# Kernel tuning notes

Measured on AMD Instinct MI355X. Metric: run time of the kernel, lower is better.

The kernel has to match this reference:

```python
import jax, jax.numpy as jnp
import numpy as np
import math

M, N, D = 16384, 8192, 128
SIGMA = 1.0

def setup_inputs() -> dict:
    key = jax.random.key(0)
    k1, k2, k3 = jax.random.split(key, 3)
    x = jax.random.normal(k1, (M, D), dtype=jnp.float32)
    means = jax.random.normal(k2, (N, D), dtype=jnp.float32)
    weights = jax.random.uniform(k3, (N,), dtype=jnp.float32)
    return {"x": x, "means": means, "weights": weights}

def reference(x, means, weights):
    # GMM.eval_batch: cdist -> square -> gaussian kernel -> weighted sum
    var = SIGMA ** 2
    x = x.reshape(-1, means.shape[-1])
    x2 = jnp.sum(x * x, axis=-1, keepdims=True)            # (M,1)
    m2 = jnp.sum(means * means, axis=-1)                   # (N,)
    sq = jnp.maximum(x2 + m2[None, :] - 2.0 * (x @ means.T), 0.0)  # (M,N)
    coef = 1.0 / (2.0 * math.pi * var)
    dens = coef * jnp.exp(-sq / (2.0 * var))               # (M,N)
    return dens @ weights                                  # (M,)
```

## Files before the change

### kernel.cpp

```cpp
#include <hip/hip_runtime.h>
#include <math.h>

#define MM 16384
#define NN 8192
#define DD 128

#define L2E  1.4426950408889634f
#define COEF 0.15915494309189535f

__device__ __forceinline__ unsigned short f2h(float f) {
    _Float16 h = (_Float16)f;
    unsigned short u;
    __builtin_memcpy(&u, &h, 2);
    return u;
}

__device__ __forceinline__ void async16(short* lds, const short* g) {
    __builtin_amdgcn_global_load_lds(
        (const __attribute__((address_space(1))) unsigned int*)g,
        (__attribute__((address_space(3))) unsigned int*)lds,
        16, 0, 0);
}

typedef __attribute__((ext_vector_type(8))) _Float16 f16x8;
typedef __attribute__((ext_vector_type(4))) float f32x4;

__global__ __launch_bounds__(256) void gmm_prep_f16(
    const float* __restrict__ x, const float* __restrict__ means,
    const float* __restrict__ w, short* __restrict__ Acat,
    short* __restrict__ Bcat, float* __restrict__ xc, float* __restrict__ mc)
{
    const int tid  = threadIdx.x;
    const int rbk  = blockIdx.x;
    const bool isx = rbk < (MM / 16);
    const int rb   = isx ? rbk : rbk - (MM / 16);
    const int lane = tid & 63;
    const int rp   = (tid >> 6) * 4 + (lane >> 4);
    const int cg   = lane & 15;
    const int p    = cg >> 2;
    const int gk   = cg & 3;
    const int row  = rb * 16 + rp;

    const float* src = (isx ? x : means) + (size_t)row * DD + cg * 8;
    float4 u0 = ((const float4*)src)[0];
    float4 u1 = ((const float4*)src)[1];
    float a[8] = {u0.x, u0.y, u0.z, u0.w, u1.x, u1.y, u1.z, u1.w};

    float ss = 0.f;
    unsigned hi[4];
    #pragma unroll
    for (int q = 0; q < 4; ++q) {
        ss = fmaf(a[2 * q], a[2 * q], fmaf(a[2 * q + 1], a[2 * q + 1], ss));
        float a0 = isx ? a[2 * q] * L2E     : a[2 * q];
        float a1 = isx ? a[2 * q + 1] * L2E : a[2 * q + 1];
        hi[q] = (unsigned)f2h(a0) | ((unsigned)f2h(a1) << 16);
    }
    uint4 HI = make_uint4(hi[0], hi[1], hi[2], hi[3]);

    const int slot = rp * 4 + ((gk + (rp >> 1)) & 3);
    short* base = (isx ? Acat : Bcat) + (size_t)rb * 2048 + p * 512 + slot * 8;
    *(uint4*)base = HI;

    ss += __shfl_xor(ss, 1, 16);
    ss += __shfl_xor(ss, 2, 16);
    ss += __shfl_xor(ss, 4, 16);
    ss += __shfl_xor(ss, 8, 16);
    if (cg == 0) {
        if (isx) xc[row] = -0.5f * ss * L2E;
        else     mc[row] = (logf(w[row]) - 0.5f * ss) * L2E;
    }
}

__global__ __launch_bounds__(512, 4) void gmm_mfma(
    const short* __restrict__ Acat, const short* __restrict__ Bcat,
    const float* __restrict__ xc, const float* __restrict__ mc,
    float* __restrict__ out)
{
    __shared__ __align__(16) short smem[36864];
    __shared__ float red[4][128];

#define AS(b) (smem + (b) * 4096)
#define BS(b) (smem + 12288 + (b) * 8192)

    const int tid  = threadIdx.x;
    const int w    = tid >> 6, lane = tid & 63;
    const int wm   = w >> 2,   wn   = w & 3;
    const int quad = lane >> 4, col = lane & 15;
    const int m0   = blockIdx.x * 128;
    const int nb   = blockIdx.y * 256;

    const short* ga  = Acat + (size_t)(blockIdx.x * 8 + w) * 2048 + lane * 8;
    const short* gb0 = Bcat + (size_t)(blockIdx.y * 16 + w * 2) * 2048 + lane * 8;
    const short* gb1 = gb0 + 2048;
    const int aofs  = w * 512;
    const int bofs0 = w * 1024;
    const int bofs1 = w * 1024 + 512;

    float mcv[4];
    #pragma unroll
    for (int j = 0; j < 4; ++j) mcv[j] = mc[nb + wn * 64 + j * 16 + col];
    float xa[4][4];
    #pragma unroll
    for (int i = 0; i < 4; ++i) {
        float4 xv = *(const float4*)(xc + m0 + wm * 64 + i * 16 + quad * 4);
        xa[i][0] = xv.x; xa[i][1] = xv.y; xa[i][2] = xv.z; xa[i][3] = xv.w;
    }

    f32x4 acc[4][4];
    #pragma unroll
    for (int i = 0; i < 4; ++i)
        #pragma unroll
        for (int j = 0; j < 4; ++j)
            acc[i][j] = (f32x4){xa[i][0] + mcv[j], xa[i][1] + mcv[j],
                                xa[i][2] + mcv[j], xa[i][3] + mcv[j]};

    asm volatile("s_waitcnt vmcnt(0)" ::: "memory");
    __builtin_amdgcn_sched_barrier(0);

    async16(AS(0) + aofs,  ga);
    async16(BS(0) + bofs0, gb0);
    async16(BS(0) + bofs1, gb1);
    async16(AS(1) + aofs,  ga  + 512);
    async16(BS(1) + bofs0, gb0 + 512);
    async16(BS(1) + bofs1, gb1 + 512);

    const int rdo = col * 32 + ((quad + (col >> 1)) & 3) * 8;

#define COMPUTE(as_, bs_)                                                     \
    {                                                                         \
        const short* as = (as_);                                              \
        const short* bs = (bs_);                                              \
        f16x8 af[4];                                                          \
        _Pragma("unroll")                                                     \
        for (int i = 0; i < 4; ++i)                                           \
            af[i] = *(const f16x8*)(as + (wm * 4 + i) * 512 + rdo);           \
        _Pragma("unroll")                                                     \
        for (int j = 0; j < 4; ++j) {                                         \
            f16x8 bfr = *(const f16x8*)(&bs[(wn * 4 + j) * 512 + rdo]);       \
            _Pragma("unroll")                                                 \
            for (int i = 0; i < 4; ++i)                                       \
                acc[i][j] = __builtin_amdgcn_mfma_f32_16x16x32_f16(           \
                    af[i], bfr, acc[i][j], 0, 0, 0);                          \
        }                                                                     \
    }

    asm volatile("s_waitcnt vmcnt(3)" ::: "memory");
    __builtin_amdgcn_sched_barrier(0);
    __builtin_amdgcn_s_barrier();
    __builtin_amdgcn_sched_barrier(0);
    async16(AS(2) + aofs,  ga  + 1024);
    async16(BS(2) + bofs0, gb0 + 1024);
    async16(BS(2) + bofs1, gb1 + 1024);
    COMPUTE(AS(0), BS(0));

    asm volatile("s_waitcnt vmcnt(3)" ::: "memory");
    __builtin_amdgcn_sched_barrier(0);
    __builtin_amdgcn_s_barrier();
    __builtin_amdgcn_sched_barrier(0);
    async16(AS(0) + aofs,  ga  + 1536);
    async16(BS(0) + bofs0, gb0 + 1536);
    async16(BS(0) + bofs1, gb1 + 1536);
    COMPUTE(AS(1), BS(1));

    asm volatile("s_waitcnt vmcnt(3)" ::: "memory");
    __builtin_amdgcn_sched_barrier(0);
    __builtin_amdgcn_s_barrier();
    __builtin_amdgcn_sched_barrier(0);
    COMPUTE(AS(2), BS(2));

    asm volatile("s_waitcnt vmcnt(0)" ::: "memory");
    __builtin_amdgcn_sched_barrier(0);
    __builtin_amdgcn_s_barrier();
    __builtin_amdgcn_sched_barrier(0);
    COMPUTE(AS(0), BS(0));
#undef COMPUTE

    float sv[4][4];
    #pragma unroll
    for (int i = 0; i < 4; ++i) {
        #pragma unroll
        for (int r = 0; r < 4; ++r) {
            float s = 0.f;
            #pragma unroll
            for (int j = 0; j < 4; ++j)
                s += __builtin_exp2f(acc[i][j][r]);
            sv[i][r] = s;
        }
    }
    __syncthreads();
    {
        float* S = (float*)smem;
        const int p = wn * 16 + col;
        #pragma unroll
        for (int i = 0; i < 4; ++i) {
            const int mb = wm * 64 + i * 16 + quad * 4;
            #pragma unroll
            for (int r = 0; r < 4; ++r)
                S[(mb + r) * 68 + p] = sv[i][r];
        }
    }
    __syncthreads();
    {
        const float* S = (const float*)smem;
        const int m  = tid & 127;
        const int pg = tid >> 7;
        const float4* v = (const float4*)(S + m * 68 + pg * 16);
        float4 a0 = v[0], a1 = v[1], a2 = v[2], a3 = v[3];
        red[pg][m] = (a0.x + a0.y + a0.z + a0.w) + (a1.x + a1.y + a1.z + a1.w)
                   + (a2.x + a2.y + a2.z + a2.w) + (a3.x + a3.y + a3.z + a3.w);
    }
    __syncthreads();
    if (tid < 128)
        atomicAdd(out + m0 + tid,
                  COEF * (red[0][tid] + red[1][tid] + red[2][tid] + red[3][tid]));
#undef AS
#undef BS
}

__global__ __launch_bounds__(256) void gmm_prep(
    const float* __restrict__ x, const float* __restrict__ means,
    const float* __restrict__ w, float* __restrict__ xc, float* __restrict__ mc)
{
    int tid = blockIdx.x * 256 + threadIdx.x;
    if (tid < MM) {
        const float4* row = (const float4*)(x + (size_t)tid * DD);
        float ss = 0.f;
        #pragma unroll
        for (int i = 0; i < DD / 4; ++i) {
            float4 v = row[i];
            ss = fmaf(v.x, v.x, fmaf(v.y, v.y, fmaf(v.z, v.z, fmaf(v.w, v.w, ss))));
        }
        xc[tid] = -0.5f * ss * L2E;
    } else if (tid < MM + NN) {
        int n = tid - MM;
        const float4* row = (const float4*)(means + (size_t)n * DD);
        float ss = 0.f;
        #pragma unroll
        for (int i = 0; i < DD / 4; ++i) {
            float4 v = row[i];
            ss = fmaf(v.x, v.x, fmaf(v.y, v.y, fmaf(v.z, v.z, fmaf(v.w, v.w, ss))));
        }
        mc[n] = (logf(w[n]) - 0.5f * ss) * L2E;
    }
}

__global__ __launch_bounds__(256, 2) void gmm_main(
    const float* __restrict__ x, const float* __restrict__ means,
    const float* __restrict__ xc, const float* __restrict__ mc,
    float* __restrict__ out)
{
    __shared__ __align__(16) float Asm[128 * 128];
    __shared__ __align__(16) float Bsm[2][16 * 128];

    const int t   = threadIdx.x;
    const int tc  = t & 15;
    const int tr  = t >> 4;
    const int r0  = blockIdx.x * 128;
    const int nq0 = blockIdx.y * 2048;

    {
        float4 tmp[16];
        #pragma unroll
        for (int ii = 0; ii < 16; ++ii) {
            int idx = t + ii * 256;
            int r   = idx >> 5;
            int k0  = (idx & 31) << 2;
            tmp[ii] = *(const float4*)(x + (size_t)(r0 + r) * DD + k0);
        }
        #pragma unroll
        for (int ii = 0; ii < 16; ++ii) {
            int idx = t + ii * 256;
            int r   = idx >> 5;
            int k0  = (idx & 31) << 2;
            int rb  = r >> 3, rl = r & 7;
            float v[4] = {tmp[ii].x, tmp[ii].y, tmp[ii].z, tmp[ii].w};
            #pragma unroll
            for (int j = 0; j < 4; ++j) {
                int k = k0 + j;
                Asm[k * 128 + (((rb ^ (k & 15)) << 3) | rl)] = v[j];
            }
        }
    }

    float xcv[8];
    {
        float4 a = *(const float4*)(xc + r0 + tr * 8);
        float4 b = *(const float4*)(xc + r0 + tr * 8 + 4);
        xcv[0] = a.x; xcv[1] = a.y; xcv[2] = a.z; xcv[3] = a.w;
        xcv[4] = b.x; xcv[5] = b.y; xcv[6] = b.z; xcv[7] = b.w;
    }

    float rowAcc[8];
    #pragma unroll
    for (int i = 0; i < 8; ++i) rowAcc[i] = 0.f;

    for (int ntile = 0; ntile < 16; ++ntile) {
        const int nbase = nq0 + ntile * 128;

        float acc[8][8];
        #pragma unroll
        for (int i = 0; i < 8; ++i)
            #pragma unroll
            for (int j = 0; j < 8; ++j) acc[i][j] = 0.f;

        float4 ld[2];
        #pragma unroll
        for (int ii = 0; ii < 2; ++ii) {
            int flat = t + ii * 256;
            int nl   = flat >> 2;
            int kl   = (flat & 3) << 2;
            ld[ii] = *(const float4*)(means + (size_t)(nbase + nl) * DD + kl);
        }

        for (int ks = 0; ks < 8; ++ks) {
            const int buf = ks & 1;
            #pragma unroll
            for (int ii = 0; ii < 2; ++ii) {
                int flat = t + ii * 256;
                int nl   = flat >> 2;
                int k0   = (flat & 3) << 2;
                int nbk  = nl >> 3, nll = nl & 7;
                float v[4] = {ld[ii].x, ld[ii].y, ld[ii].z, ld[ii].w};
                #pragma unroll
                for (int j = 0; j < 4; ++j) {
                    int kl = k0 + j;
                    Bsm[buf][kl * 128 + (((nbk ^ kl) << 3) | nll)] = v[j];
                }
            }
            if (ks < 7) {
                #pragma unroll
                for (int ii = 0; ii < 2; ++ii) {
                    int flat = t + ii * 256;
                    int nl   = flat >> 2;
                    int kl   = (flat & 3) << 2;
                    ld[ii] = *(const float4*)(means + (size_t)(nbase + nl) * DD
                                              + (ks + 1) * 16 + kl);
                }
            }
            __syncthreads();

            #pragma unroll
            for (int kk = 0; kk < 16; ++kk) {
                const int k = ks * 16 + kk;
                const float* apx = &Asm[k * 128 + ((tr ^ kk) << 3)];
                float4 a0 = *(const float4*)apx;
                float4 a1 = *(const float4*)(apx + 4);
                const float* bpx = &Bsm[buf][kk * 128 + ((tc ^ kk) << 3)];
                float4 b0 = *(const float4*)bpx;
                float4 b1 = *(const float4*)(bpx + 4);
                float av[8] = {a0.x, a0.y, a0.z, a0.w, a1.x, a1.y, a1.z, a1.w};
                float bv[8] = {b0.x, b0.y, b0.z, b0.w, b1.x, b1.y, b1.z, b1.w};
                #pragma unroll
                for (int i = 0; i < 8; ++i)
                    #pragma unroll
                    for (int j = 0; j < 8; ++j)
                        acc[i][j] = fmaf(av[i], bv[j], acc[i][j]);
            }
        }

        float mcv[8];
        {
            float4 a = *(const float4*)(mc + nbase + tc * 8);
            float4 b = *(const float4*)(mc + nbase + tc * 8 + 4);
            mcv[0] = a.x; mcv[1] = a.y; mcv[2] = a.z; mcv[3] = a.w;
            mcv[4] = b.x; mcv[5] = b.y; mcv[6] = b.z; mcv[7] = b.w;
        }
        #pragma unroll
        for (int i = 0; i < 8; ++i) {
            float s = 0.f;
            #pragma unroll
            for (int j = 0; j < 8; ++j) {
                float arg = fmaf(acc[i][j], L2E, xcv[i] + mcv[j]);
                s += __builtin_exp2f(arg);
            }
            rowAcc[i] += s;
        }
    }

    #pragma unroll
    for (int i = 0; i < 8; ++i) {
        float v = rowAcc[i];
        v += __shfl_xor(v, 1, 16);
        v += __shfl_xor(v, 2, 16);
        v += __shfl_xor(v, 4, 16);
        v += __shfl_xor(v, 8, 16);
        if (tc == 0) atomicAdd(out + r0 + tr * 8 + i, COEF * v);
    }
}

extern "C" void kernel_launch(void* const* d_in, const int* in_sizes, int n_in,
                              void* d_out, int out_size, void* d_ws, size_t ws_size,
                              hipStream_t stream) {
    const float* x     = (const float*)d_in[0];
    const float* means = (const float*)d_in[1];
    const float* w     = (const float*)d_in[2];
    float* out = (float*)d_out;

    const size_t needA = (size_t)MM * 128 * sizeof(short);
    const size_t needB = (size_t)NN * 128 * sizeof(short);
    const size_t need  = needA + needB + (size_t)(MM + NN) * 4;

    if (ws_size >= need) {
        short* Acat = (short*)d_ws;
        short* Bcat = Acat + (size_t)MM * 128;
        float* xc   = (float*)(Bcat + (size_t)NN * 128);
        float* mc   = xc + MM;
        hipMemsetAsync(out, 0, MM * sizeof(float), stream);
        gmm_prep_f16<<<(MM + NN) / 16, 256, 0, stream>>>(x, means, w, Acat, Bcat, xc, mc);
        gmm_mfma<<<dim3(MM / 128, NN / 256), 512, 0, stream>>>(Acat, Bcat, xc, mc, out);
    } else {
        float* xc = (float*)d_ws;
        float* mc = xc + MM;
        hipMemsetAsync(out, 0, MM * sizeof(float), stream);
        gmm_prep<<<(MM + NN + 255) / 256, 256, 0, stream>>>(x, means, w, xc, mc);
        gmm_main<<<dim3(MM / 128, 4), 256, 0, stream>>>(x, means, xc, mc, out);
    }
}
```

Baseline: 123.3 us.

## Shrink MFMA block tile to 128x128 with 256 threads and 4 waves

Changes the fused GEMM-exp kernel from a 128x256 tile with 8 waves to a 128x128 tile with 4 waves, so each wave now loads two A and two B chunks per stage. LDS use per block drops, the grid doubles along N, and the reduction is adjusted to two partial groups. The aim is more resident blocks per CU and better latency hiding. In exchange, B-tile reuse per block is lower, global and L2 traffic for A rises, and twice as many atomics go to the output.

```diff
diff --git a/kernel.cpp b/kernel.cpp
--- a/kernel.cpp
+++ b/kernel.cpp
@@ -71,30 +71,30 @@
     }
 }
 
-__global__ __launch_bounds__(512, 4) void gmm_mfma(
+__global__ __launch_bounds__(256, 3) void gmm_mfma(
     const short* __restrict__ Acat, const short* __restrict__ Bcat,
     const float* __restrict__ xc, const float* __restrict__ mc,
     float* __restrict__ out)
 {
-    __shared__ __align__(16) short smem[36864];
-    __shared__ float red[4][128];
+    __shared__ __align__(16) short smem[24576];
+    __shared__ float red[2][128];
 
 #define AS(b) (smem + (b) * 4096)
-#define BS(b) (smem + 12288 + (b) * 8192)
+#define BS(b) (smem + 12288 + (b) * 4096)
 
     const int tid  = threadIdx.x;
     const int w    = tid >> 6, lane = tid & 63;
-    const int wm   = w >> 2,   wn   = w & 3;
+    const int wm   = w >> 1,   wn   = w & 1;
     const int quad = lane >> 4, col = lane & 15;
     const int m0   = blockIdx.x * 128;
-    const int nb   = blockIdx.y * 256;
-
-    const short* ga  = Acat + (size_t)(blockIdx.x * 8 + w) * 2048 + lane * 8;
-    const short* gb0 = Bcat + (size_t)(blockIdx.y * 16 + w * 2) * 2048 + lane * 8;
+    const int nb   = blockIdx.y * 128;
+
+    const short* ga0 = Acat + (size_t)(blockIdx.x * 8 + w * 2) * 2048 + lane * 8;
+    const short* ga1 = ga0 + 2048;
+    const short* gb0 = Bcat + (size_t)(blockIdx.y * 8 + w * 2) * 2048 + lane * 8;
     const short* gb1 = gb0 + 2048;
-    const int aofs  = w * 512;
-    const int bofs0 = w * 1024;
-    const int bofs1 = w * 1024 + 512;
+    const int ofs0 = w * 1024;
+    const int ofs1 = w * 1024 + 512;
 
     float mcv[4];
     #pragma unroll
@@ -117,14 +117,22 @@
     asm volatile("s_waitcnt vmcnt(0)" ::: "memory");
     __builtin_amdgcn_sched_barrier(0);
 
-    async16(AS(0) + aofs,  ga);
-    async16(BS(0) + bofs0, gb0);
-    async16(BS(0) + bofs1, gb1);
-    async16(AS(1) + aofs,  ga  + 512);
-    async16(BS(1) + bofs0, gb0 + 512);
-    async16(BS(1) + bofs1, gb1 + 512);
+    async16(AS(0) + ofs0, ga0);
+    async16(AS(0) + ofs1, ga1);
+    async16(BS(0) + ofs0, gb0);
+    async16(BS(0) + ofs1, gb1);
+    async16(AS(1) + ofs0, ga0 + 512);
+    async16(AS(1) + ofs1, ga1 + 512);
+    async16(BS(1) + ofs0, gb0 + 512);
+    async16(BS(1) + ofs1, gb1 + 512);
 
     const int rdo = col * 32 + ((quad + (col >> 1)) & 3) * 8;
+
+#define ISSUE(G, B)                                                           \
+    async16(AS(B) + ofs0, ga0 + (G) * 512);                                   \
+    async16(AS(B) + ofs1, ga1 + (G) * 512);                                   \
+    async16(BS(B) + ofs0, gb0 + (G) * 512);                                   \
+    async16(BS(B) + ofs1, gb1 + (G) * 512);
 
 #define COMPUTE(as_, bs_)                                                     \
     {                                                                         \
@@ -144,25 +152,21 @@
         }                                                                     \
     }
 
-    asm volatile("s_waitcnt vmcnt(3)" ::: "memory");
+    asm volatile("s_waitcnt vmcnt(4)" ::: "memory");
     __builtin_amdgcn_sched_barrier(0);
     __builtin_amdgcn_s_barrier();
     __builtin_amdgcn_sched_barrier(0);
-    async16(AS(2) + aofs,  ga  + 1024);
-    async16(BS(2) + bofs0, gb0 + 1024);
-    async16(BS(2) + bofs1, gb1 + 1024);
+    ISSUE(2, 2)
     COMPUTE(AS(0), BS(0));
 
-    asm volatile("s_waitcnt vmcnt(3)" ::: "memory");
+    asm volatile("s_waitcnt vmcnt(4)" ::: "memory");
     __builtin_amdgcn_sched_barrier(0);
     __builtin_amdgcn_s_barrier();
     __builtin_amdgcn_sched_barrier(0);
-    async16(AS(0) + aofs,  ga  + 1536);
-    async16(BS(0) + bofs0, gb0 + 1536);
-    async16(BS(0) + bofs1, gb1 + 1536);
+    ISSUE(3, 0)
     COMPUTE(AS(1), BS(1));
 
-    asm volatile("s_waitcnt vmcnt(3)" ::: "memory");
+    asm volatile("s_waitcnt vmcnt(4)" ::: "memory");
     __builtin_amdgcn_sched_barrier(0);
     __builtin_amdgcn_s_barrier();
     __builtin_amdgcn_sched_barrier(0);
@@ -173,6 +177,7 @@
     __builtin_amdgcn_s_barrier();
     __builtin_amdgcn_sched_barrier(0);
     COMPUTE(AS(0), BS(0));
+#undef ISSUE
 #undef COMPUTE
 
     float sv[4][4];
@@ -196,7 +201,7 @@
             const int mb = wm * 64 + i * 16 + quad * 4;
             #pragma unroll
             for (int r = 0; r < 4; ++r)
-                S[(mb + r) * 68 + p] = sv[i][r];
+                S[(mb + r) * 36 + p] = sv[i][r];
         }
     }
     __syncthreads();
@@ -204,15 +209,14 @@
         const float* S = (const float*)smem;
         const int m  = tid & 127;
         const int pg = tid >> 7;
-        const float4* v = (const float4*)(S + m * 68 + pg * 16);
+        const float4* v = (const float4*)(S + m * 36 + pg * 16);
         float4 a0 = v[0], a1 = v[1], a2 = v[2], a3 = v[3];
         red[pg][m] = (a0.x + a0.y + a0.z + a0.w) + (a1.x + a1.y + a1.z + a1.w)
                    + (a2.x + a2.y + a2.z + a2.w) + (a3.x + a3.y + a3.z + a3.w);
     }
     __syncthreads();
     if (tid < 128)
-        atomicAdd(out + m0 + tid,
-                  COEF * (red[0][tid] + red[1][tid] + red[2][tid] + red[3][tid]));
+        atomicAdd(out + m0 + tid, COEF * (red[0][tid] + red[1][tid]));
 #undef AS
 #undef BS
 }
@@ -407,7 +411,7 @@
         float* mc   = xc + MM;
         hipMemsetAsync(out, 0, MM * sizeof(float), stream);
         gmm_prep_f16<<<(MM + NN) / 16, 256, 0, stream>>>(x, means, w, Acat, Bcat, xc, mc);
-        gmm_mfma<<<dim3(MM / 128, NN / 256), 512, 0, stream>>>(Acat, Bcat, xc, mc, out);
+        gmm_mfma<<<dim3(MM / 128, NN / 128), 256, 0, stream>>>(Acat, Bcat, xc, mc, out);
     } else {
         float* xc = (float*)d_ws;
         float* mc = xc + MM;
```

Measured after the change: 124.8 us. Within noise of the previous version (+1.3%).
